# Kernel optimization log

Hardware: AMD Instinct MI355X
Metric: run time of the kernel (lower is better)

Reference implementation:

```python
import jax, jax.numpy as jnp
import numpy as np

B, S, D = 16, 2048, 256
SCALE = 1.0 / np.sqrt(D).astype(np.float32)

def setup_inputs() -> dict:
    key = jax.random.key(0)
    k1, k2, k3, k4 = jax.random.split(key, 4)
    x = jax.random.normal(k1, (B, S, D), dtype=jnp.float32)
    w_qkv = jax.random.normal(k2, (3 * D, D), dtype=jnp.float32) * (1.0 / np.sqrt(D))
    w_out = jax.random.normal(k3, (D, D), dtype=jnp.float32) * (1.0 / np.sqrt(D))
    b_out = jax.random.normal(k4, (D,), dtype=jnp.float32) * 0.01
    return {"x": x, "w_qkv": w_qkv, "w_out": w_out, "b_out": b_out}

def reference(x, w_qkv, w_out, b_out):
    # qkv: [B, S, 3D] = x @ W_qkv^T (torch Linear convention)
    qkv = jnp.einsum('bsd,ed->bse', x, w_qkv)
    q, k, v = jnp.split(qkv, 3, axis=-1)  # each [B, S, D]
    scores = jnp.einsum('bsd,btd->bst', q, k) * SCALE  # [B, S, S]
    attn = jax.nn.softmax(scores, axis=-1)  # dropout = identity (eval mode)
    ctx = jnp.einsum('bst,btd->bsd', attn, v)  # [B, S, D]
    out = jnp.einsum('bsd,ed->bse', ctx, w_out) + b_out
    return out
```

## Files before the change

kernel.cpp:

```cpp
#include <hip/hip_runtime.h>
#include <hip/hip_bf16.h>


typedef short bf16x8 __attribute__((ext_vector_type(8)));
typedef float f32x4 __attribute__((ext_vector_type(4)));

#define MFMA16(a, b, c) __builtin_amdgcn_mfma_f32_16x16x32_bf16((a), (b), (c), 0, 0, 0)

__device__ __forceinline__ unsigned short f2bf(float f) {
  unsigned int x;
  __builtin_memcpy(&x, &f, 4);
  x = x + 0x7fffu + ((x >> 16) & 1u);
  return (unsigned short)(x >> 16);
}
__device__ __forceinline__ unsigned int pack2(float a, float b) {
  float2 t;
  t.x = a;
  t.y = b;
  __hip_bfloat162 h = __float22bfloat162_rn(t);
  unsigned int u;
  __builtin_memcpy(&u, &h, 4);
  return u;
}

typedef __attribute__((address_space(3))) void as3_void;
typedef __attribute__((address_space(1))) const void as1_void;
__device__ __forceinline__ void gl_lds16(const void* g, void* l) {
  __builtin_amdgcn_global_load_lds((as1_void*)(unsigned long long)g,
                                   (as3_void*)(unsigned int)(unsigned long long)l,
                                   16, 0, 0);
}

__global__ __launch_bounds__(256, 4) void cvtw_kernel(
    const float* __restrict__ W, unsigned short* __restrict__ Wbf) {
  int idx = blockIdx.x * 256 + threadIdx.x;
  int row = idx >> 5, sc = idx & 31;
  int c = (sc & 24) | ((sc ^ (row & 7)) & 7);
  const float* wp = W + (size_t)row * 256 + c * 8;
  float4 a0 = *(const float4*)wp, a1 = *(const float4*)(wp + 4);
  uint4 u;
  u.x = pack2(a0.x, a0.y);
  u.y = pack2(a0.z, a0.w);
  u.z = pack2(a1.x, a1.y);
  u.w = pack2(a1.z, a1.w);
  *(uint4*)(Wbf + (size_t)idx * 8) = u;
}

__global__ __launch_bounds__(256, 2) void qkv_kernel(
    const float* __restrict__ X, const unsigned short* __restrict__ Wqbf,
    unsigned short* __restrict__ Q, unsigned short* __restrict__ Kp,
    unsigned short* __restrict__ Vt) {
  __shared__ unsigned short Al[64 * 256];
  __shared__ unsigned short Bl[64 * 256];
  const int m0 = blockIdx.x * 64;
  const int t = threadIdx.x;
  const int w = t >> 6, lane = t & 63, lo = lane & 15, quad = lane >> 4;
  const int wr = (w >> 1) * 32, wc = (w & 1) * 32;

#pragma unroll
  for (int r = 0; r < 8; ++r) {
    int ci = r * 256 + t;
    int row = ci >> 5, c = ci & 31;
    int s = (c & 24) | ((c ^ (row & 7)) & 7);
    const float* xp = X + (size_t)(m0 + row) * 256 + c * 8;
    float4 a0 = *(const float4*)xp, a1 = *(const float4*)(xp + 4);
    uint4 ua;
    ua.x = pack2(a0.x, a0.y);
    ua.y = pack2(a0.z, a0.w);
    ua.z = pack2(a1.x, a1.y);
    ua.w = pack2(a1.z, a1.w);
    *(uint4*)(&Al[row * 256 + s * 8]) = ua;
  }

  const int lofs = __builtin_amdgcn_readfirstlane(w * 64 * 8);
  for (int n = 0; n < 12; ++n) {
    const int n0 = n * 64;
    if (n > 0) __syncthreads();
    {
      const unsigned short* Wb = Wqbf + (size_t)n0 * 256;
#pragma unroll
      for (int r = 0; r < 8; ++r)
        gl_lds16(Wb + (size_t)(r * 256 + t) * 8, &Bl[r * 256 * 8 + lofs]);
    }
    asm volatile("s_waitcnt vmcnt(0)" ::: "memory");
    __syncthreads();

    f32x4 zero4 = {0.f, 0.f, 0.f, 0.f};
    f32x4 acc[2][2];
#pragma unroll
    for (int i = 0; i < 2; i++)
#pragma unroll
      for (int j = 0; j < 2; j++) acc[i][j] = zero4;

#pragma unroll
    for (int kc = 0; kc < 8; ++kc) {
      const int c = kc * 4 + quad;
      const int jj = (c & 24) | ((c ^ (lo & 7)) & 7);
      bf16x8 af[2], bfr[2];
#pragma unroll
      for (int mt = 0; mt < 2; ++mt)
        af[mt] = *(const bf16x8*)(&Al[(wr + mt * 16 + lo) * 256 + jj * 8]);
#pragma unroll
      for (int nt = 0; nt < 2; ++nt)
        bfr[nt] = *(const bf16x8*)(&Bl[(wc + nt * 16 + lo) * 256 + jj * 8]);
#pragma unroll
      for (int mt = 0; mt < 2; ++mt)
#pragma unroll
        for (int nt = 0; nt < 2; ++nt)
          acc[mt][nt] = MFMA16(af[mt], bfr[nt], acc[mt][nt]);
    }

    const int mb = m0 + wr, nb = n0 + wc;
    if (n0 < 256) {
#pragma unroll
      for (int mt = 0; mt < 2; ++mt)
#pragma unroll
        for (int nt = 0; nt < 2; ++nt) {
          int m = mb + mt * 16 + quad * 4;
          int nn = nb + nt * 16 + lo;
          unsigned short* p = Q + (size_t)m * 256 + nn;
          p[0] = f2bf(acc[mt][nt][0]);
          p[256] = f2bf(acc[mt][nt][1]);
          p[512] = f2bf(acc[mt][nt][2]);
          p[768] = f2bf(acc[mt][nt][3]);
        }
    } else if (n0 < 512) {
#pragma unroll
      for (int mt = 0; mt < 2; ++mt)
#pragma unroll
        for (int nt = 0; nt < 2; ++nt) {
          int m = mb + mt * 16 + quad * 4;
          int nn = nb + nt * 16 + lo - 256;
          unsigned short* p = Kp + (size_t)m * 256 + nn;
          p[0] = f2bf(acc[mt][nt][0]);
          p[256] = f2bf(acc[mt][nt][1]);
          p[512] = f2bf(acc[mt][nt][2]);
          p[768] = f2bf(acc[mt][nt][3]);
        }
    } else {
#pragma unroll
      for (int mt = 0; mt < 2; ++mt)
#pragma unroll
        for (int nt = 0; nt < 2; ++nt) {
          int m = mb + mt * 16 + quad * 4;
          int d = nb + nt * 16 + lo - 512;
          int b = m >> 11, s = m & 2047;
          uint2 v;
          v.x = pack2(acc[mt][nt][0], acc[mt][nt][1]);
          v.y = pack2(acc[mt][nt][2], acc[mt][nt][3]);
          *(uint2*)(Vt + ((size_t)(b * 256 + d)) * 2048 + s) = v;
        }
    }
  }
}

__global__ __launch_bounds__(512, 2) void attn_kernel(
    const unsigned short* __restrict__ Q, const unsigned short* __restrict__ K,
    const unsigned short* __restrict__ Vt, const float* __restrict__ Wo,
    const float* __restrict__ bias, float* __restrict__ out) {
  __shared__ __attribute__((aligned(16))) unsigned short smem[65536];
  const int id = blockIdx.x;
  const int b = id & 15;
  const int qt = id >> 4;
  const int t = threadIdx.x;
  const int w = t >> 6, lane = t & 63, lo = lane & 15, quad = lane >> 4;
  constexpr float SCALE_LOG2E = 0.0625f * 1.4426950408889634f;

  const unsigned short* Kb = K + (size_t)b * 2048 * 256;
  const unsigned short* Vb = Vt + (size_t)b * 256 * 2048;

  unsigned int gkoff[4], gvoff[4];
  int loK[4], loV[4];
#pragma unroll
  for (int r = 0; r < 4; ++r) {
    int ck = r * 512 + t;
    int row = ck >> 5, j = ck & 31;
    int srcj = (j & 16) | ((j ^ (row & 15)) & 15);
    gkoff[r] = (unsigned int)((row * 256 + srcj * 8) * 2);
    loK[r] = __builtin_amdgcn_readfirstlane((r * 512 + w * 64) * 8);

    int cv = r * 512 + t;
    int d = cv >> 3, slot = cv & 7;
    int g = slot ^ (d & 7);
    gvoff[r] = (unsigned int)((d * 2048 + g * 8) * 2);
    loV[r] = __builtin_amdgcn_readfirstlane(16384 + (r * 512 + w * 64) * 8);
  }

  const int qrow = b * 2048 + qt * 128 + w * 16 + lo;
  const unsigned short* qp = Q + (size_t)qrow * 256;
  bf16x8 qf[8];
#pragma unroll
  for (int ks = 0; ks < 8; ++ks)
    qf[ks] = *(const bf16x8*)(qp + ks * 32 + quad * 8);

  f32x4 zero4 = {0.f, 0.f, 0.f, 0.f};
  f32x4 oacc[16];
#pragma unroll
  for (int i = 0; i < 16; i++) oacc[i] = zero4;
  float m_run = -1e30f, l_run = 0.f;

#pragma unroll
  for (int r = 0; r < 4; ++r) {
    gl_lds16((const char*)Kb + gkoff[r], &smem[loK[r]]);
    gkoff[r] += 64 * 256 * 2;
  }
#pragma unroll
  for (int r = 0; r < 4; ++r) {
    gl_lds16((const char*)Vb + gvoff[r], &smem[loV[r]]);
    gvoff[r] += 64 * 2;
  }

  for (int it = 0; it < 32; ++it) {
    asm volatile("s_waitcnt vmcnt(0)" ::: "memory");
    __syncthreads();
    if (it < 31) {
      const int pn = ((it + 1) & 1) * 32768;
#pragma unroll
      for (int r = 0; r < 4; ++r) {
        gl_lds16((const char*)Kb + gkoff[r], &smem[pn + loK[r]]);
        gkoff[r] += 64 * 256 * 2;
      }
#pragma unroll
      for (int r = 0; r < 4; ++r) {
        gl_lds16((const char*)Vb + gvoff[r], &smem[pn + loV[r]]);
        gvoff[r] += 64 * 2;
      }
    }
    const unsigned short* Kl = smem + (it & 1) * 32768;
    const unsigned short* Vl = Kl + 16384;

    f32x4 sacc[4];
#pragma unroll
    for (int r = 0; r < 4; ++r) sacc[r] = zero4;
    __builtin_amdgcn_s_setprio(1);
#pragma unroll
    for (int ks = 0; ks < 8; ++ks) {
      const int c = ks * 4 + quad;
      const int jj = (c & 16) | ((c ^ lo) & 15);
#pragma unroll
      for (int r = 0; r < 4; ++r) {
        bf16x8 kf = *(const bf16x8*)(&Kl[(r * 16 + lo) * 256 + jj * 8]);
        sacc[r] = MFMA16(kf, qf[ks], sacc[r]);
      }
    }
    __builtin_amdgcn_s_setprio(0);

    float p[4][4];
    float cmax = -1e30f;
#pragma unroll
    for (int r = 0; r < 4; r++)
#pragma unroll
      for (int i = 0; i < 4; i++) {
        p[r][i] = sacc[r][i] * SCALE_LOG2E;
        cmax = fmaxf(cmax, p[r][i]);
      }
    cmax = fmaxf(cmax, __shfl_xor(cmax, 16));
    cmax = fmaxf(cmax, __shfl_xor(cmax, 32));
    if (!__all(cmax <= m_run + 8.f)) {
      float mnew = fmaxf(m_run, cmax);
      float alpha = exp2f(m_run - mnew);
      l_run *= alpha;
#pragma unroll
      for (int i = 0; i < 16; i++) oacc[i] *= alpha;
      m_run = mnew;
    }
    float rsum = 0.f;
#pragma unroll
    for (int r = 0; r < 4; r++)
#pragma unroll
      for (int i = 0; i < 4; i++) {
        p[r][i] = exp2f(p[r][i] - m_run);
        rsum += p[r][i];
      }
    rsum += __shfl_xor(rsum, 16);
    rsum += __shfl_xor(rsum, 32);
    l_run += rsum;

    unsigned int pk[4][2];
#pragma unroll
    for (int r = 0; r < 4; r++) {
      pk[r][0] = pack2(p[r][0], p[r][1]);
      pk[r][1] = pack2(p[r][2], p[r][3]);
    }

#pragma unroll
    for (int ks2 = 0; ks2 < 2; ++ks2) {
      union {
        unsigned int u[4];
        bf16x8 v;
      } cvt;
#pragma unroll
      for (int dd = 0; dd < 4; ++dd) {
        int src = lo + 16 * ((2 * quad + (dd >> 1)) & 3);
        unsigned int v0 = (unsigned int)__shfl((int)pk[2 * ks2][dd & 1], src);
        unsigned int v1 = (unsigned int)__shfl((int)pk[2 * ks2 + 1][dd & 1], src);
        cvt.u[dd] = (quad >> 1) ? v1 : v0;
      }
      bf16x8 pf = cvt.v;
      __builtin_amdgcn_s_setprio(1);
#pragma unroll
      for (int dt = 0; dt < 16; ++dt) {
        int slot = (ks2 * 4 + quad) ^ (lo & 7);
        bf16x8 vf = *(const bf16x8*)(&Vl[(dt * 16 + lo) * 64 + slot * 8]);
        oacc[dt] = MFMA16(vf, pf, oacc[dt]);
      }
      __builtin_amdgcn_s_setprio(0);
    }
  }

  float inv = 1.0f / l_run;
  uint2 c2[16];
#pragma unroll
  for (int dt = 0; dt < 16; ++dt) {
    c2[dt].x = pack2(oacc[dt][0] * inv, oacc[dt][1] * inv);
    c2[dt].y = pack2(oacc[dt][2] * inv, oacc[dt][3] * inv);
  }

  __syncthreads();
#pragma unroll
  for (int r = 0; r < 16; ++r) {
    int ci = r * 512 + t;
    int row = ci >> 5, c = ci & 31;
    int s = (c & 24) | ((c ^ (row & 7)) & 7);
    const float* wp = Wo + (size_t)row * 256 + c * 8;
    float4 a0 = *(const float4*)wp, a1 = *(const float4*)(wp + 4);
    uint4 ua;
    ua.x = pack2(a0.x, a0.y);
    ua.y = pack2(a0.z, a0.w);
    ua.z = pack2(a1.x, a1.y);
    ua.w = pack2(a1.z, a1.w);
    *(uint4*)(&smem[row * 256 + s * 8]) = ua;
  }
  __syncthreads();

  f32x4 outacc[16];
#pragma unroll
  for (int i = 0; i < 16; i++) outacc[i] = zero4;

#pragma unroll
  for (int ks = 0; ks < 8; ++ks) {
    int sa = lo + 16 * ((quad & 1) * 2);
    unsigned int xA = (unsigned int)__shfl((int)c2[2 * ks].x, sa);
    unsigned int yA = (unsigned int)__shfl((int)c2[2 * ks].y, sa);
    unsigned int xB = (unsigned int)__shfl((int)c2[2 * ks].x, sa + 16);
    unsigned int yB = (unsigned int)__shfl((int)c2[2 * ks].y, sa + 16);
    unsigned int xA1 = (unsigned int)__shfl((int)c2[2 * ks + 1].x, sa);
    unsigned int yA1 = (unsigned int)__shfl((int)c2[2 * ks + 1].y, sa);
    unsigned int xB1 = (unsigned int)__shfl((int)c2[2 * ks + 1].x, sa + 16);
    unsigned int yB1 = (unsigned int)__shfl((int)c2[2 * ks + 1].y, sa + 16);
    union {
      unsigned int u[4];
      bf16x8 v;
    } cvt;
    bool hiq = (quad >> 1) != 0;
    cvt.u[0] = hiq ? xA1 : xA;
    cvt.u[1] = hiq ? yA1 : yA;
    cvt.u[2] = hiq ? xB1 : xB;
    cvt.u[3] = hiq ? yB1 : yB;
    bf16x8 pf = cvt.v;

    const int c = ks * 4 + quad;
    const int jj = (c & 24) | ((c ^ (lo & 7)) & 7);
    __builtin_amdgcn_s_setprio(1);
#pragma unroll
    for (int et = 0; et < 16; ++et) {
      bf16x8 af = *(const bf16x8*)(&smem[(et * 16 + lo) * 256 + jj * 8]);
      outacc[et] = MFMA16(af, pf, outacc[et]);
    }
    __builtin_amdgcn_s_setprio(0);
  }

  float* op = out + (size_t)qrow * 256;
#pragma unroll
  for (int et = 0; et < 16; ++et) {
    const float4 b4 = *(const float4*)(bias + et * 16 + quad * 4);
    float4 v;
    v.x = outacc[et][0] + b4.x;
    v.y = outacc[et][1] + b4.y;
    v.z = outacc[et][2] + b4.z;
    v.w = outacc[et][3] + b4.w;
    *(float4*)(op + et * 16 + quad * 4) = v;
  }
}

extern "C" void kernel_launch(void* const* d_in, const int* in_sizes, int n_in,
                              void* d_out, int out_size, void* d_ws, size_t ws_size,
                              hipStream_t stream) {
  const float* X = (const float*)d_in[0];
  const float* Wq = (const float*)d_in[1];
  const float* Wo = (const float*)d_in[2];
  const float* Bo = (const float*)d_in[3];
  float* out = (float*)d_out;
  unsigned short* ws = (unsigned short*)d_ws;

  const size_t NE = (size_t)16 * 2048 * 256;
  unsigned short* Qb = ws;
  unsigned short* Kb = ws + NE;
  unsigned short* Vt = ws + 2 * NE;
  unsigned short* Wqbf = (unsigned short*)d_out;

  cvtw_kernel<<<dim3(96), 256, 0, stream>>>(Wq, Wqbf);
  qkv_kernel<<<dim3(512), 256, 0, stream>>>(X, Wqbf, Qb, Kb, Vt);
  attn_kernel<<<dim3(256), 512, 0, stream>>>(Qb, Kb, Vt, Wo, Bo, out);
}
```

Before: 204.8 us.

## Fuse weight conversion, QKV projection and attention into one cooperative kernel

```diff
diff --git a/kernel.cpp b/kernel.cpp
--- a/kernel.cpp
+++ b/kernel.cpp
@@ -1,5 +1,8 @@
 #include <hip/hip_runtime.h>
 #include <hip/hip_bf16.h>
+#include <hip/hip_cooperative_groups.h>
+
+namespace cg = cooperative_groups;
 
 
 typedef short bf16x8 __attribute__((ext_vector_type(8)));
@@ -31,355 +34,364 @@
                                    16, 0, 0);
 }
 
-__global__ __launch_bounds__(256, 4) void cvtw_kernel(
-    const float* __restrict__ W, unsigned short* __restrict__ Wbf) {
-  int idx = blockIdx.x * 256 + threadIdx.x;
-  int row = idx >> 5, sc = idx & 31;
-  int c = (sc & 24) | ((sc ^ (row & 7)) & 7);
-  const float* wp = W + (size_t)row * 256 + c * 8;
-  float4 a0 = *(const float4*)wp, a1 = *(const float4*)(wp + 4);
-  uint4 u;
-  u.x = pack2(a0.x, a0.y);
-  u.y = pack2(a0.z, a0.w);
-  u.z = pack2(a1.x, a1.y);
-  u.w = pack2(a1.z, a1.w);
-  *(uint4*)(Wbf + (size_t)idx * 8) = u;
-}
-
-__global__ __launch_bounds__(256, 2) void qkv_kernel(
-    const float* __restrict__ X, const unsigned short* __restrict__ Wqbf,
-    unsigned short* __restrict__ Q, unsigned short* __restrict__ Kp,
-    unsigned short* __restrict__ Vt) {
-  __shared__ unsigned short Al[64 * 256];
-  __shared__ unsigned short Bl[64 * 256];
-  const int m0 = blockIdx.x * 64;
+__global__ __launch_bounds__(512, 2) void fused_kernel(
+    const float* __restrict__ X, const float* __restrict__ Wq,
+    const float* __restrict__ Wo, const float* __restrict__ bias,
+    unsigned short* __restrict__ Qb, unsigned short* __restrict__ Kb,
+    unsigned short* __restrict__ Vt, unsigned short* __restrict__ Wqbf,
+    float* __restrict__ out) {
+  __shared__ __attribute__((aligned(16))) unsigned short smem[65536];
+  cg::grid_group grid = cg::this_grid();
+
   const int t = threadIdx.x;
   const int w = t >> 6, lane = t & 63, lo = lane & 15, quad = lane >> 4;
-  const int wr = (w >> 1) * 32, wc = (w & 1) * 32;
-
-#pragma unroll
-  for (int r = 0; r < 8; ++r) {
-    int ci = r * 256 + t;
-    int row = ci >> 5, c = ci & 31;
-    int s = (c & 24) | ((c ^ (row & 7)) & 7);
-    const float* xp = X + (size_t)(m0 + row) * 256 + c * 8;
-    float4 a0 = *(const float4*)xp, a1 = *(const float4*)(xp + 4);
-    uint4 ua;
-    ua.x = pack2(a0.x, a0.y);
-    ua.y = pack2(a0.z, a0.w);
-    ua.z = pack2(a1.x, a1.y);
-    ua.w = pack2(a1.z, a1.w);
-    *(uint4*)(&Al[row * 256 + s * 8]) = ua;
+
+  {
+    int idx = blockIdx.x * 512 + t;
+    if (idx < 24576) {
+      int row = idx >> 5, sc = idx & 31;
+      int c = (sc & 24) | ((sc ^ (row & 7)) & 7);
+      const float* wp = Wq + (size_t)row * 256 + c * 8;
+      float4 a0 = *(const float4*)wp, a1 = *(const float4*)(wp + 4);
+      uint4 u;
+      u.x = pack2(a0.x, a0.y);
+      u.y = pack2(a0.z, a0.w);
+      u.z = pack2(a1.x, a1.y);
+      u.w = pack2(a1.z, a1.w);
+      *(uint4*)(Wqbf + (size_t)idx * 8) = u;
+    }
   }
-
-  const int lofs = __builtin_amdgcn_readfirstlane(w * 64 * 8);
-  for (int n = 0; n < 12; ++n) {
-    const int n0 = n * 64;
-    if (n > 0) __syncthreads();
-    {
-      const unsigned short* Wb = Wqbf + (size_t)n0 * 256;
-#pragma unroll
-      for (int r = 0; r < 8; ++r)
-        gl_lds16(Wb + (size_t)(r * 256 + t) * 8, &Bl[r * 256 * 8 + lofs]);
-    }
-    asm volatile("s_waitcnt vmcnt(0)" ::: "memory");
+  __threadfence();
+  grid.sync();
+  __threadfence();
+
+  {
+    unsigned short* Al = smem;
+    unsigned short* Bl = smem + 32768;
+    const int m0 = blockIdx.x * 128;
+    const int wr = (w >> 2) * 64, wc = (w & 3) * 32;
+
+#pragma unroll
+    for (int r = 0; r < 8; ++r) {
+      int ci = r * 512 + t;
+      int row = ci >> 5, c = ci & 31;
+      int s = (c & 24) | ((c ^ (row & 7)) & 7);
+      const float* xp = X + (size_t)(m0 + row) * 256 + c * 8;
+      float4 a0 = *(const float4*)xp, a1 = *(const float4*)(xp + 4);
+      uint4 ua;
+      ua.x = pack2(a0.x, a0.y);
+      ua.y = pack2(a0.z, a0.w);
+      ua.z = pack2(a1.x, a1.y);
+      ua.w = pack2(a1.z, a1.w);
+      *(uint4*)(&Al[row * 256 + s * 8]) = ua;
+    }
+
+    for (int n = 0; n < 6; ++n) {
+      const int n0 = n * 128;
+      if (n > 0) __syncthreads();
+      {
+        const unsigned short* Wb = Wqbf + (size_t)n0 * 256;
+        int lofs = __builtin_amdgcn_readfirstlane(w * 64 * 8);
+#pragma unroll
+        for (int r = 0; r < 8; ++r)
+          gl_lds16(Wb + (size_t)(r * 512 + t) * 8, &Bl[r * 512 * 8 + lofs]);
+      }
+      asm volatile("s_waitcnt vmcnt(0)" ::: "memory");
+      __syncthreads();
+
+      f32x4 zero4 = {0.f, 0.f, 0.f, 0.f};
+      f32x4 acc[4][2];
+#pragma unroll
+      for (int i = 0; i < 4; i++)
+#pragma unroll
+        for (int j = 0; j < 2; j++) acc[i][j] = zero4;
+
+#pragma unroll
+      for (int kc = 0; kc < 8; ++kc) {
+        const int c = kc * 4 + quad;
+        const int jj = (c & 24) | ((c ^ (lo & 7)) & 7);
+        bf16x8 af[4], bfr[2];
+#pragma unroll
+        for (int mt = 0; mt < 4; ++mt)
+          af[mt] = *(const bf16x8*)(&Al[(wr + mt * 16 + lo) * 256 + jj * 8]);
+#pragma unroll
+        for (int nt = 0; nt < 2; ++nt)
+          bfr[nt] = *(const bf16x8*)(&Bl[(wc + nt * 16 + lo) * 256 + jj * 8]);
+#pragma unroll
+        for (int mt = 0; mt < 4; ++mt)
+#pragma unroll
+          for (int nt = 0; nt < 2; ++nt)
+            acc[mt][nt] = MFMA16(af[mt], bfr[nt], acc[mt][nt]);
+      }
+
+      const int mb = m0 + wr, nb = n0 + wc;
+      if (n0 < 256) {
+#pragma unroll
+        for (int mt = 0; mt < 4; ++mt)
+#pragma unroll
+          for (int nt = 0; nt < 2; ++nt) {
+            int m = mb + mt * 16 + quad * 4;
+            int nn = nb + nt * 16 + lo;
+            unsigned short* p = Qb + (size_t)m * 256 + nn;
+            p[0] = f2bf(acc[mt][nt][0]);
+            p[256] = f2bf(acc[mt][nt][1]);
+            p[512] = f2bf(acc[mt][nt][2]);
+            p[768] = f2bf(acc[mt][nt][3]);
+          }
+      } else if (n0 < 512) {
+#pragma unroll
+        for (int mt = 0; mt < 4; ++mt)
+#pragma unroll
+          for (int nt = 0; nt < 2; ++nt) {
+            int m = mb + mt * 16 + quad * 4;
+            int nn = nb + nt * 16 + lo - 256;
+            unsigned short* p = Kb + (size_t)m * 256 + nn;
+            p[0] = f2bf(acc[mt][nt][0]);
+            p[256] = f2bf(acc[mt][nt][1]);
+            p[512] = f2bf(acc[mt][nt][2]);
+            p[768] = f2bf(acc[mt][nt][3]);
+          }
+      } else {
+#pragma unroll
+        for (int mt = 0; mt < 4; ++mt)
+#pragma unroll
+          for (int nt = 0; nt < 2; ++nt) {
+            int m = mb + mt * 16 + quad * 4;
+            int d = nb + nt * 16 + lo - 512;
+            int b = m >> 11, s = m & 2047;
+            uint2 v;
+            v.x = pack2(acc[mt][nt][0], acc[mt][nt][1]);
+            v.y = pack2(acc[mt][nt][2], acc[mt][nt][3]);
+            *(uint2*)(Vt + ((size_t)(b * 256 + d)) * 2048 + s) = v;
+          }
+      }
+    }
+  }
+  __threadfence();
+  grid.sync();
+  __threadfence();
+
+  {
+    const int id = blockIdx.x;
+    const int b = id & 15;
+    const int qt = id >> 4;
+    constexpr float SCALE_LOG2E = 0.0625f * 1.4426950408889634f;
+
+    const unsigned short* Kbb = Kb + (size_t)b * 2048 * 256;
+    const unsigned short* Vb = Vt + (size_t)b * 256 * 2048;
+
+    unsigned int gkoff[4], gvoff[4];
+    int loK[4], loV[4];
+#pragma unroll
+    for (int r = 0; r < 4; ++r) {
+      int ck = r * 512 + t;
+      int row = ck >> 5, j = ck & 31;
+      int srcj = (j & 16) | ((j ^ (row & 15)) & 15);
+      gkoff[r] = (unsigned int)((row * 256 + srcj * 8) * 2);
+      loK[r] = __builtin_amdgcn_readfirstlane((r * 512 + w * 64) * 8);
+
+      int cv = r * 512 + t;
+      int d = cv >> 3, slot = cv & 7;
+      int g = slot ^ (d & 7);
+      gvoff[r] = (unsigned int)((d * 2048 + g * 8) * 2);
+      loV[r] = __builtin_amdgcn_readfirstlane(16384 + (r * 512 + w * 64) * 8);
+    }
+
+    const int qrow = b * 2048 + qt * 128 + w * 16 + lo;
+    const unsigned short* qp = Qb + (size_t)qrow * 256;
+    bf16x8 qf[8];
+#pragma unroll
+    for (int ks = 0; ks < 8; ++ks)
+      qf[ks] = *(const bf16x8*)(qp + ks * 32 + quad * 8);
+
+    f32x4 zero4 = {0.f, 0.f, 0.f, 0.f};
+    f32x4 oacc[16];
+#pragma unroll
+    for (int i = 0; i < 16; i++) oacc[i] = zero4;
+    float m_run = -1e30f, l_run = 0.f;
+
+#pragma unroll
+    for (int r = 0; r < 4; ++r) {
+      gl_lds16((const char*)Kbb + gkoff[r], &smem[loK[r]]);
+      gkoff[r] += 64 * 256 * 2;
+    }
+#pragma unroll
+    for (int r = 0; r < 4; ++r) {
+      gl_lds16((const char*)Vb + gvoff[r], &smem[loV[r]]);
+      gvoff[r] += 64 * 2;
+    }
+
+    for (int it = 0; it < 32; ++it) {
+      asm volatile("s_waitcnt vmcnt(0)" ::: "memory");
+      __syncthreads();
+      if (it < 31) {
+        const int pn = ((it + 1) & 1) * 32768;
+#pragma unroll
+        for (int r = 0; r < 4; ++r) {
+          gl_lds16((const char*)Kbb + gkoff[r], &smem[pn + loK[r]]);
+          gkoff[r] += 64 * 256 * 2;
+        }
+#pragma unroll
+        for (int r = 0; r < 4; ++r) {
+          gl_lds16((const char*)Vb + gvoff[r], &smem[pn + loV[r]]);
+          gvoff[r] += 64 * 2;
+        }
+      }
+      const unsigned short* Kl = smem + (it & 1) * 32768;
+      const unsigned short* Vl = Kl + 16384;
+
+      f32x4 sacc[4];
+#pragma unroll
+      for (int r = 0; r < 4; ++r) sacc[r] = zero4;
+      __builtin_amdgcn_s_setprio(1);
+#pragma unroll
+      for (int ks = 0; ks < 8; ++ks) {
+        const int c = ks * 4 + quad;
+        const int jj = (c & 16) | ((c ^ lo) & 15);
+#pragma unroll
+        for (int r = 0; r < 4; ++r) {
+          bf16x8 kf = *(const bf16x8*)(&Kl[(r * 16 + lo) * 256 + jj * 8]);
+          sacc[r] = MFMA16(kf, qf[ks], sacc[r]);
+        }
+      }
+      __builtin_amdgcn_s_setprio(0);
+
+      float p[4][4];
+      float cmax = -1e30f;
+#pragma unroll
+      for (int r = 0; r < 4; r++)
+#pragma unroll
+        for (int i = 0; i < 4; i++) {
+          p[r][i] = sacc[r][i] * SCALE_LOG2E;
+          cmax = fmaxf(cmax, p[r][i]);
+        }
+      cmax = fmaxf(cmax, __shfl_xor(cmax, 16));
+      cmax = fmaxf(cmax, __shfl_xor(cmax, 32));
+      if (!__all(cmax <= m_run + 8.f)) {
+        float mnew = fmaxf(m_run, cmax);
+        float alpha = exp2f(m_run - mnew);
+        l_run *= alpha;
+#pragma unroll
+        for (int i = 0; i < 16; i++) oacc[i] *= alpha;
+        m_run = mnew;
+      }
+      float rsum = 0.f;
+#pragma unroll
+      for (int r = 0; r < 4; r++)
+#pragma unroll
+        for (int i = 0; i < 4; i++) {
+          p[r][i] = exp2f(p[r][i] - m_run);
+          rsum += p[r][i];
+        }
+      rsum += __shfl_xor(rsum, 16);
+      rsum += __shfl_xor(rsum, 32);
+      l_run += rsum;
+
+      unsigned int pk[4][2];
+#pragma unroll
+      for (int r = 0; r < 4; r++) {
+        pk[r][0] = pack2(p[r][0], p[r][1]);
+        pk[r][1] = pack2(p[r][2], p[r][3]);
+      }
+
+#pragma unroll
+      for (int ks2 = 0; ks2 < 2; ++ks2) {
+        union {
+          unsigned int u[4];
+          bf16x8 v;
+        } cvt;
+#pragma unroll
+        for (int dd = 0; dd < 4; ++dd) {
+          int src = lo + 16 * ((2 * quad + (dd >> 1)) & 3);
+          unsigned int v0 = (unsigned int)__shfl((int)pk[2 * ks2][dd & 1], src);
+          unsigned int v1 = (unsigned int)__shfl((int)pk[2 * ks2 + 1][dd & 1], src);
+          cvt.u[dd] = (quad >> 1) ? v1 : v0;
+        }
+        bf16x8 pf = cvt.v;
+        __builtin_amdgcn_s_setprio(1);
+#pragma unroll
+        for (int dt = 0; dt < 16; ++dt) {
+          int slot = (ks2 * 4 + quad) ^ (lo & 7);
+          bf16x8 vf = *(const bf16x8*)(&Vl[(dt * 16 + lo) * 64 + slot * 8]);
+          oacc[dt] = MFMA16(vf, pf, oacc[dt]);
+        }
+        __builtin_amdgcn_s_setprio(0);
+      }
+    }
+
+    float inv = 1.0f / l_run;
+    uint2 c2[16];
+#pragma unroll
+    for (int dt = 0; dt < 16; ++dt) {
+      c2[dt].x = pack2(oacc[dt][0] * inv, oacc[dt][1] * inv);
+      c2[dt].y = pack2(oacc[dt][2] * inv, oacc[dt][3] * inv);
+    }
+
     __syncthreads();
-
-    f32x4 zero4 = {0.f, 0.f, 0.f, 0.f};
-    f32x4 acc[2][2];
-#pragma unroll
-    for (int i = 0; i < 2; i++)
-#pragma unroll
-      for (int j = 0; j < 2; j++) acc[i][j] = zero4;
-
-#pragma unroll
-    for (int kc = 0; kc < 8; ++kc) {
-      const int c = kc * 4 + quad;
-      const int jj = (c & 24) | ((c ^ (lo & 7)) & 7);
-      bf16x8 af[2], bfr[2];
-#pragma unroll
-      for (int mt = 0; mt < 2; ++mt)
-        af[mt] = *(const bf16x8*)(&Al[(wr + mt * 16 + lo) * 256 + jj * 8]);
-#pragma unroll
-      for (int nt = 0; nt < 2; ++nt)
-        bfr[nt] = *(const bf16x8*)(&Bl[(wc + nt * 16 + lo) * 256 + jj * 8]);
-#pragma unroll
-      for (int mt = 0; mt < 2; ++mt)
-#pragma unroll
-        for (int nt = 0; nt < 2; ++nt)
-          acc[mt][nt] = MFMA16(af[mt], bfr[nt], acc[mt][nt]);
-    }
-
-    const int mb = m0 + wr, nb = n0 + wc;
-    if (n0 < 256) {
-#pragma unroll
-      for (int mt = 0; mt < 2; ++mt)
-#pragma unroll
-        for (int nt = 0; nt < 2; ++nt) {
-          int m = mb + mt * 16 + quad * 4;
-          int nn = nb + nt * 16 + lo;
-          unsigned short* p = Q + (size_t)m * 256 + nn;
-          p[0] = f2bf(acc[mt][nt][0]);
-          p[256] = f2bf(acc[mt][nt][1]);
-          p[512] = f2bf(acc[mt][nt][2]);
-          p[768] = f2bf(acc[mt][nt][3]);
-        }
-    } else if (n0 < 512) {
-#pragma unroll
-      for (int mt = 0; mt < 2; ++mt)
-#pragma unroll
-        for (int nt = 0; nt < 2; ++nt) {
-          int m = mb + mt * 16 + quad * 4;
-          int nn = nb + nt * 16 + lo - 256;
-          unsigned short* p = Kp + (size_t)m * 256 + nn;
-          p[0] = f2bf(acc[mt][nt][0]);
-          p[256] = f2bf(acc[mt][nt][1]);
-          p[512] = f2bf(acc[mt][nt][2]);
-          p[768] = f2bf(acc[mt][nt][3]);
-        }
-    } else {
-#pragma unroll
-      for (int mt = 0; mt < 2; ++mt)
-#pragma unroll
-        for (int nt = 0; nt < 2; ++nt) {
-          int m = mb + mt * 16 + quad * 4;
-          int d = nb + nt * 16 + lo - 512;
-          int b = m >> 11, s = m & 2047;
-          uint2 v;
-          v.x = pack2(acc[mt][nt][0], acc[mt][nt][1]);
-          v.y = pack2(acc[mt][nt][2], acc[mt][nt][3]);
-          *(uint2*)(Vt + ((size_t)(b * 256 + d)) * 2048 + s) = v;
-        }
-    }
-  }
-}
-
-__global__ __launch_bounds__(512, 2) void attn_kernel(
-    const unsigned short* __restrict__ Q, const unsigned short* __restrict__ K,
-    const unsigned short* __restrict__ Vt, const float* __restrict__ Wo,
-    const float* __restrict__ bias, float* __restrict__ out) {
-  __shared__ __attribute__((aligned(16))) unsigned short smem[65536];
-  const int id = blockIdx.x;
-  const int b = id & 15;
-  const int qt = id >> 4;
-  const int t = threadIdx.x;
-  const int w = t >> 6, lane = t & 63, lo = lane & 15, quad = lane >> 4;
-  constexpr float SCALE_LOG2E = 0.0625f * 1.4426950408889634f;
-
-  const unsigned short* Kb = K + (size_t)b * 2048 * 256;
-  const unsigned short* Vb = Vt + (size_t)b * 256 * 2048;
-
-  unsigned int gkoff[4], gvoff[4];
-  int loK[4], loV[4];
-#pragma unroll
-  for (int r = 0; r < 4; ++r) {
-    int ck = r * 512 + t;
-    int row = ck >> 5, j = ck & 31;
-    int srcj = (j & 16) | ((j ^ (row & 15)) & 15);
-    gkoff[r] = (unsigned int)((row * 256 + srcj * 8) * 2);
-    loK[r] = __builtin_amdgcn_readfirstlane((r * 512 + w * 64) * 8);
-
-    int cv = r * 512 + t;
-    int d = cv >> 3, slot = cv & 7;
-    int g = slot ^ (d & 7);
-    gvoff[r] = (unsigned int)((d * 2048 + g * 8) * 2);
-    loV[r] = __builtin_amdgcn_readfirstlane(16384 + (r * 512 + w * 64) * 8);
-  }
-
-  const int qrow = b * 2048 + qt * 128 + w * 16 + lo;
-  const unsigned short* qp = Q + (size_t)qrow * 256;
-  bf16x8 qf[8];
-#pragma unroll
-  for (int ks = 0; ks < 8; ++ks)
-    qf[ks] = *(const bf16x8*)(qp + ks * 32 + quad * 8);
-
-  f32x4 zero4 = {0.f, 0.f, 0.f, 0.f};
-  f32x4 oacc[16];
-#pragma unroll
-  for (int i = 0; i < 16; i++) oacc[i] = zero4;
-  float m_run = -1e30f, l_run = 0.f;
-
-#pragma unroll
-  for (int r = 0; r < 4; ++r) {
-    gl_lds16((const char*)Kb + gkoff[r], &smem[loK[r]]);
-    gkoff[r] += 64 * 256 * 2;
-  }
-#pragma unroll
-  for (int r = 0; r < 4; ++r) {
-    gl_lds16((const char*)Vb + gvoff[r], &smem[loV[r]]);
-    gvoff[r] += 64 * 2;
-  }
-
-  for (int it = 0; it < 32; ++it) {
-    asm volatile("s_waitcnt vmcnt(0)" ::: "memory");
+#pragma unroll
+    for (int r = 0; r < 16; ++r) {
+      int ci = r * 512 + t;
+      int row = ci >> 5, c = ci & 31;
+      int s = (c & 24) | ((c ^ (row & 7)) & 7);
+      const float* wp = Wo + (size_t)row * 256 + c * 8;
+      float4 a0 = *(const float4*)wp, a1 = *(const float4*)(wp + 4);
+      uint4 ua;
+      ua.x = pack2(a0.x, a0.y);
+      ua.y = pack2(a0.z, a0.w);
+      ua.z = pack2(a1.x, a1.y);
+      ua.w = pack2(a1.z, a1.w);
+      *(uint4*)(&smem[row * 256 + s * 8]) = ua;
+    }
     __syncthreads();
-    if (it < 31) {
-      const int pn = ((it + 1) & 1) * 32768;
-#pragma unroll
-      for (int r = 0; r < 4; ++r) {
-        gl_lds16((const char*)Kb + gkoff[r], &smem[pn + loK[r]]);
-        gkoff[r] += 64 * 256 * 2;
-      }
-#pragma unroll
-      for (int r = 0; r < 4; ++r) {
-        gl_lds16((const char*)Vb + gvoff[r], &smem[pn + loV[r]]);
-        gvoff[r] += 64 * 2;
-      }
-    }
-    const unsigned short* Kl = smem + (it & 1) * 32768;
-    const unsigned short* Vl = Kl + 16384;
-
-    f32x4 sacc[4];
-#pragma unroll
-    for (int r = 0; r < 4; ++r) sacc[r] = zero4;
-    __builtin_amdgcn_s_setprio(1);
+
+    f32x4 outacc[16];
+#pragma unroll
+    for (int i = 0; i < 16; i++) outacc[i] = zero4;
+
 #pragma unroll
     for (int ks = 0; ks < 8; ++ks) {
-      const int c = ks * 4 + quad;
-      const int jj = (c & 16) | ((c ^ lo) & 15);
-#pragma unroll
-      for (int r = 0; r < 4; ++r) {
-        bf16x8 kf = *(const bf16x8*)(&Kl[(r * 16 + lo) * 256 + jj * 8]);
-        sacc[r] = MFMA16(kf, qf[ks], sacc[r]);
-      }
-    }
-    __builtin_amdgcn_s_setprio(0);
-
-    float p[4][4];
-    float cmax = -1e30f;
-#pragma unroll
-    for (int r = 0; r < 4; r++)
-#pragma unroll
-      for (int i = 0; i < 4; i++) {
-        p[r][i] = sacc[r][i] * SCALE_LOG2E;
-        cmax = fmaxf(cmax, p[r][i]);
-      }
-    cmax = fmaxf(cmax, __shfl_xor(cmax, 16));
-    cmax = fmaxf(cmax, __shfl_xor(cmax, 32));
-    if (!__all(cmax <= m_run + 8.f)) {
-      float mnew = fmaxf(m_run, cmax);
-      float alpha = exp2f(m_run - mnew);
-      l_run *= alpha;
-#pragma unroll
-      for (int i = 0; i < 16; i++) oacc[i] *= alpha;
-      m_run = mnew;
-    }
-    float rsum = 0.f;
-#pragma unroll
-    for (int r = 0; r < 4; r++)
-#pragma unroll
-      for (int i = 0; i < 4; i++) {
-        p[r][i] = exp2f(p[r][i] - m_run);
-        rsum += p[r][i];
-      }
-    rsum += __shfl_xor(rsum, 16);
-    rsum += __shfl_xor(rsum, 32);
-    l_run += rsum;
-
-    unsigned int pk[4][2];
-#pragma unroll
-    for (int r = 0; r < 4; r++) {
-      pk[r][0] = pack2(p[r][0], p[r][1]);
-      pk[r][1] = pack2(p[r][2], p[r][3]);
-    }
-
-#pragma unroll
-    for (int ks2 = 0; ks2 < 2; ++ks2) {
+      int sa = lo + 16 * ((quad & 1) * 2);
+      unsigned int xA = (unsigned int)__shfl((int)c2[2 * ks].x, sa);
+      unsigned int yA = (unsigned int)__shfl((int)c2[2 * ks].y, sa);
+      unsigned int xB = (unsigned int)__shfl((int)c2[2 * ks].x, sa + 16);
+      unsigned int yB = (unsigned int)__shfl((int)c2[2 * ks].y, sa + 16);
+      unsigned int xA1 = (unsigned int)__shfl((int)c2[2 * ks + 1].x, sa);
+      unsigned int yA1 = (unsigned int)__shfl((int)c2[2 * ks + 1].y, sa);
+      unsigned int xB1 = (unsigned int)__shfl((int)c2[2 * ks + 1].x, sa + 16);
+      unsigned int yB1 = (unsigned int)__shfl((int)c2[2 * ks + 1].y, sa + 16);
       union {
         unsigned int u[4];
         bf16x8 v;
       } cvt;
-#pragma unroll
-      for (int dd = 0; dd < 4; ++dd) {
-        int src = lo + 16 * ((2 * quad + (dd >> 1)) & 3);
-        unsigned int v0 = (unsigned int)__shfl((int)pk[2 * ks2][dd & 1], src);
-        unsigned int v1 = (unsigned int)__shfl((int)pk[2 * ks2 + 1][dd & 1], src);
-        cvt.u[dd] = (quad >> 1) ? v1 : v0;
-      }
+      bool hiq = (quad >> 1) != 0;
+      cvt.u[0] = hiq ? xA1 : xA;
+      cvt.u[1] = hiq ? yA1 : yA;
+      cvt.u[2] = hiq ? xB1 : xB;
+      cvt.u[3] = hiq ? yB1 : yB;
       bf16x8 pf = cvt.v;
+
+      const int c = ks * 4 + quad;
+      const int jj = (c & 24) | ((c ^ (lo & 7)) & 7);
       __builtin_amdgcn_s_setprio(1);
 #pragma unroll
-      for (int dt = 0; dt < 16; ++dt) {
-        int slot = (ks2 * 4 + quad) ^ (lo & 7);
-        bf16x8 vf = *(const bf16x8*)(&Vl[(dt * 16 + lo) * 64 + slot * 8]);
-        oacc[dt] = MFMA16(vf, pf, oacc[dt]);
+      for (int et = 0; et < 16; ++et) {
+        bf16x8 af = *(const bf16x8*)(&smem[(et * 16 + lo) * 256 + jj * 8]);
+        outacc[et] = MFMA16(af, pf, outacc[et]);
       }
       __builtin_amdgcn_s_setprio(0);
     }
-  }
-
-  float inv = 1.0f / l_run;
-  uint2 c2[16];
-#pragma unroll
-  for (int dt = 0; dt < 16; ++dt) {
-    c2[dt].x = pack2(oacc[dt][0] * inv, oacc[dt][1] * inv);
-    c2[dt].y = pack2(oacc[dt][2] * inv, oacc[dt][3] * inv);
-  }
-
-  __syncthreads();
-#pragma unroll
-  for (int r = 0; r < 16; ++r) {
-    int ci = r * 512 + t;
-    int row = ci >> 5, c = ci & 31;
-    int s = (c & 24) | ((c ^ (row & 7)) & 7);
-    const float* wp = Wo + (size_t)row * 256 + c * 8;
-    float4 a0 = *(const float4*)wp, a1 = *(const float4*)(wp + 4);
-    uint4 ua;
-    ua.x = pack2(a0.x, a0.y);
-    ua.y = pack2(a0.z, a0.w);
-    ua.z = pack2(a1.x, a1.y);
-    ua.w = pack2(a1.z, a1.w);
-    *(uint4*)(&smem[row * 256 + s * 8]) = ua;
-  }
-  __syncthreads();
-
-  f32x4 outacc[16];
-#pragma unroll
-  for (int i = 0; i < 16; i++) outacc[i] = zero4;
-
-#pragma unroll
-  for (int ks = 0; ks < 8; ++ks) {
-    int sa = lo + 16 * ((quad & 1) * 2);
-    unsigned int xA = (unsigned int)__shfl((int)c2[2 * ks].x, sa);
-    unsigned int yA = (unsigned int)__shfl((int)c2[2 * ks].y, sa);
-    unsigned int xB = (unsigned int)__shfl((int)c2[2 * ks].x, sa + 16);
-    unsigned int yB = (unsigned int)__shfl((int)c2[2 * ks].y, sa + 16);
-    unsigned int xA1 = (unsigned int)__shfl((int)c2[2 * ks + 1].x, sa);
-    unsigned int yA1 = (unsigned int)__shfl((int)c2[2 * ks + 1].y, sa);
-    unsigned int xB1 = (unsigned int)__shfl((int)c2[2 * ks + 1].x, sa + 16);
-    unsigned int yB1 = (unsigned int)__shfl((int)c2[2 * ks + 1].y, sa + 16);
-    union {
-      unsigned int u[4];
-      bf16x8 v;
-    } cvt;
-    bool hiq = (quad >> 1) != 0;
-    cvt.u[0] = hiq ? xA1 : xA;
-    cvt.u[1] = hiq ? yA1 : yA;
-    cvt.u[2] = hiq ? xB1 : xB;
-    cvt.u[3] = hiq ? yB1 : yB;
-    bf16x8 pf = cvt.v;
-
-    const int c = ks * 4 + quad;
-    const int jj = (c & 24) | ((c ^ (lo & 7)) & 7);
-    __builtin_amdgcn_s_setprio(1);
+
+    float* op = out + (size_t)qrow * 256;
 #pragma unroll
     for (int et = 0; et < 16; ++et) {
-      bf16x8 af = *(const bf16x8*)(&smem[(et * 16 + lo) * 256 + jj * 8]);
-      outacc[et] = MFMA16(af, pf, outacc[et]);
-    }
-    __builtin_amdgcn_s_setprio(0);
-  }
-
-  float* op = out + (size_t)qrow * 256;
-#pragma unroll
-  for (int et = 0; et < 16; ++et) {
-    const float4 b4 = *(const float4*)(bias + et * 16 + quad * 4);
-    float4 v;
-    v.x = outacc[et][0] + b4.x;
-    v.y = outacc[et][1] + b4.y;
-    v.z = outacc[et][2] + b4.z;
-    v.w = outacc[et][3] + b4.w;
-    *(float4*)(op + et * 16 + quad * 4) = v;
+      const float4 b4 = *(const float4*)(bias + et * 16 + quad * 4);
+      float4 v;
+      v.x = outacc[et][0] + b4.x;
+      v.y = outacc[et][1] + b4.y;
+      v.z = outacc[et][2] + b4.z;
+      v.w = outacc[et][3] + b4.w;
+      *(float4*)(op + et * 16 + quad * 4) = v;
+    }
   }
 }
 
@@ -399,7 +411,8 @@
   unsigned short* Vt = ws + 2 * NE;
   unsigned short* Wqbf = (unsigned short*)d_out;
 
-  cvtw_kernel<<<dim3(96), 256, 0, stream>>>(Wq, Wqbf);
-  qkv_kernel<<<dim3(512), 256, 0, stream>>>(X, Wqbf, Qb, Kb, Vt);
-  attn_kernel<<<dim3(256), 512, 0, stream>>>(Qb, Kb, Vt, Wo, Bo, out);
+  void* args[] = {(void*)&X,  (void*)&Wq, (void*)&Wo,   (void*)&Bo, (void*)&Qb,
+                  (void*)&Kb, (void*)&Vt, (void*)&Wqbf, (void*)&out};
+  hipLaunchCooperativeKernel((const void*)fused_kernel, dim3(256), dim3(512),
+                             args, 0, stream);
 }
```

Measured after the change: 456.7 us. 2.23x slower.
